# Performance work log

Hardware: AMD Instinct MI355X
Metric: run time of the kernel (lower is better)

## Reference

```python
import jax, jax.numpy as jnp
import numpy as np

N = 100000      # nodes
E = 400000      # edges per relation
R = 4           # relations
D_IN, D_HID, D_OUT = 256, 256, 128


def setup_inputs() -> dict:
    key = jax.random.key(0)
    ks = jax.random.split(key, 6)
    x = jax.random.normal(ks[0], (N, D_IN), jnp.float32)
    src = jax.random.randint(ks[1], (R, E), 0, N)
    dst = jax.random.randint(ks[2], (R, E), 0, N)
    # glorot-ish init for per-relation GraphConv weights
    W1 = jax.random.normal(ks[3], (R, D_IN, D_HID), jnp.float32) * (1.0 / np.sqrt(D_IN))
    b1 = jnp.zeros((R, D_HID), jnp.float32)
    W2 = jax.random.normal(ks[4], (R, D_HID, D_OUT), jnp.float32) * (1.0 / np.sqrt(D_HID))
    b2 = jnp.zeros((R, D_OUT), jnp.float32)
    return {"x": x, "src": src, "dst": dst, "W1": W1, "b1": b1, "W2": W2, "b2": b2}


def _rel_graphconv(x, src, dst, W, b):
    """DGL GraphConv with norm='both': D_dst^{-1/2} A D_src^{-1/2} X W + b.
    x: [N, din]; src/dst: [E]; W: [din, dout]; b: [dout]."""
    n = x.shape[0]
    xw = x @ W                                                   # [N, dout]
    ones = jnp.ones(src.shape, jnp.float32)
    out_deg = jnp.maximum(jax.ops.segment_sum(ones, src, num_segments=n), 1.0)
    in_deg = jnp.maximum(jax.ops.segment_sum(ones, dst, num_segments=n), 1.0)
    msg = xw[src] * (out_deg[src] ** -0.5)[:, None]              # [E, dout] gather + src-norm
    agg = jax.ops.segment_sum(msg, dst, num_segments=n)          # [N, dout] scatter-add
    return agg * (in_deg ** -0.5)[:, None] + b


def _hetero_layer(x, src, dst, W, b):
    # HeteroGraphConv(aggregate='sum'): run GraphConv per relation, sum results.
    conv = jax.vmap(_rel_graphconv, in_axes=(None, 0, 0, 0, 0))
    return jnp.sum(conv(x, src, dst, W, b), axis=0)              # [N, dout]


def reference(x, src, dst, W1, b1, W2, b2):
    h = jax.nn.relu(_hetero_layer(x, src, dst, W1, b1))
    return _hetero_layer(h, src, dst, W2, b2)
```

## Files before the change

### kernel.cpp

```cpp
#include <hip/hip_runtime.h>


#define RELS 4
#define DIN 256
#define DHID 256
#define DOUT 128

typedef short short8 __attribute__((ext_vector_type(8)));
typedef unsigned short ushort8 __attribute__((ext_vector_type(8)));
typedef float f32x4 __attribute__((ext_vector_type(4)));
typedef unsigned int uint4v __attribute__((ext_vector_type(4)));


__device__ __forceinline__ unsigned short f2bf(float f) {
    unsigned int u = __float_as_uint(f);
    u += 0x7FFFu + ((u >> 16) & 1u);
    return (unsigned short)(u >> 16);
}
__device__ __forceinline__ unsigned int cvt_pk_bf16(float lo, float hi) {
    unsigned int r;
    asm("v_cvt_pk_bf16_f32 %0, %1, %2" : "=v"(r) : "v"(lo), "v"(hi));
    return r;
}


__global__ void hist_kernel(const int* __restrict__ src, const int* __restrict__ dst,
                            int* __restrict__ cnt_src, int* __restrict__ cnt_dst,
                            int* __restrict__ rank, int E, int N) {
    int i = blockIdx.x * blockDim.x + threadIdx.x;
    int j = i * 4;
    if (j >= RELS * E) return;
    int4 sv = *(const int4*)(src + j);
    int4 dv = *(const int4*)(dst + j);
    int r0 = j / E, r1 = (j + 1) / E, r2 = (j + 2) / E, r3 = (j + 3) / E;
    atomicAdd(cnt_src + (size_t)r0 * N + sv.x, 1);
    atomicAdd(cnt_src + (size_t)r1 * N + sv.y, 1);
    atomicAdd(cnt_src + (size_t)r2 * N + sv.z, 1);
    atomicAdd(cnt_src + (size_t)r3 * N + sv.w, 1);
    int rk0 = atomicAdd(cnt_dst + (size_t)r0 * N + dv.x, 1);
    int rk1 = atomicAdd(cnt_dst + (size_t)r1 * N + dv.y, 1);
    int rk2 = atomicAdd(cnt_dst + (size_t)r2 * N + dv.z, 1);
    int rk3 = atomicAdd(cnt_dst + (size_t)r3 * N + dv.w, 1);
    *(int4*)(rank + j) = make_int4(rk0, rk1, rk2, rk3);
}

__global__ void scan_norm(const int* __restrict__ counts, int* __restrict__ out,
                          int* __restrict__ blk_sums, int n, int SB,
                          const int* __restrict__ cnt, float* __restrict__ nrm, long nnorm) {
    if ((int)blockIdx.x < SB) {
        __shared__ int sh[256];
        int i = blockIdx.x * 256 + threadIdx.x;
        int v = (i < n) ? counts[i] : 0;
        sh[threadIdx.x] = v;
        __syncthreads();
#pragma unroll
        for (int off = 1; off < 256; off <<= 1) {
            int t = (threadIdx.x >= off) ? sh[threadIdx.x - off] : 0;
            __syncthreads();
            sh[threadIdx.x] += t;
            __syncthreads();
        }
        if (i < n) out[i] = sh[threadIdx.x] - v;
        if (threadIdx.x == 255) blk_sums[blockIdx.x] = sh[255];
    } else {
        long i = (long)(blockIdx.x - SB) * 256 + threadIdx.x;
        if (i < nnorm) nrm[i] = rsqrtf(fmaxf((float)cnt[i], 1.0f));
    }
}

__global__ void scan_sums(int* __restrict__ bs, int nb) {
    __shared__ int sh[256];
    __shared__ int carry;
    if (threadIdx.x == 0) carry = 0;
    __syncthreads();
    for (int base = 0; base < nb; base += 256) {
        int i = base + threadIdx.x;
        int v = (i < nb) ? bs[i] : 0;
        sh[threadIdx.x] = v;
        __syncthreads();
#pragma unroll
        for (int off = 1; off < 256; off <<= 1) {
            int t = (threadIdx.x >= off) ? sh[threadIdx.x - off] : 0;
            __syncthreads();
            sh[threadIdx.x] += t;
            __syncthreads();
        }
        if (i < nb) bs[i] = sh[threadIdx.x] - v + carry;
        int tot = sh[255];
        __syncthreads();
        if (threadIdx.x == 255) carry += tot;
        __syncthreads();
    }
}

__global__ void scan_add(int* __restrict__ out, const int* __restrict__ blk_sums,
                         int n, int total) {
    int i = blockIdx.x * 256 + threadIdx.x;
    if (i < n) out[i] += blk_sums[blockIdx.x];
    if (i == n - 1) out[n] = total;
}

__global__ void fill_kernel(const int* __restrict__ src, const int* __restrict__ dst,
                            const float* __restrict__ nsrc, const int* __restrict__ row_ptr,
                            const int* __restrict__ rank, int2* __restrict__ e_pack,
                            int E, int N) {
    int i = blockIdx.x * blockDim.x + threadIdx.x;
    int j = i * 4;
    if (j >= RELS * E) return;
    int4 sv = *(const int4*)(src + j);
    int4 dv = *(const int4*)(dst + j);
    int4 rk = *(const int4*)(rank + j);
    int r0 = j / E, r1 = (j + 1) / E, r2 = (j + 2) / E, r3 = (j + 3) / E;
    int pos0 = row_ptr[(size_t)r0 * N + dv.x] + rk.x;
    int pos1 = row_ptr[(size_t)r1 * N + dv.y] + rk.y;
    int pos2 = row_ptr[(size_t)r2 * N + dv.z] + rk.z;
    int pos3 = row_ptr[(size_t)r3 * N + dv.w] + rk.w;
    e_pack[pos0] = make_int2(sv.x, __float_as_int(nsrc[(size_t)r0 * N + sv.x]));
    e_pack[pos1] = make_int2(sv.y, __float_as_int(nsrc[(size_t)r1 * N + sv.y]));
    e_pack[pos2] = make_int2(sv.z, __float_as_int(nsrc[(size_t)r2 * N + sv.z]));
    e_pack[pos3] = make_int2(sv.w, __float_as_int(nsrc[(size_t)r3 * N + sv.w]));
}


__global__ void prep_fused(const float* __restrict__ x, const float* __restrict__ W1,
                           const float* __restrict__ W2, const float* __restrict__ b1,
                           const float* __restrict__ b2,
                           unsigned short* __restrict__ x_bf, unsigned short* __restrict__ w1t,
                           unsigned short* __restrict__ w2t,
                           float* __restrict__ b1s, float* __restrict__ b2s,
                           int4* __restrict__ cnt_zero, long nz, long n8x) {
    const int T1 = RELS * DIN * DHID;
    const int T2 = RELS * DHID * DOUT;
    long i = blockIdx.x * (long)blockDim.x + threadIdx.x;
    if (i < nz) {
        cnt_zero[i] = make_int4(0, 0, 0, 0);
        return;
    }
    i -= nz;
    if (i < n8x) {
        const float4* ip = (const float4*)(x + i * 8);
        float4 v0 = ip[0], v1 = ip[1];
        ushort4 o0 = make_ushort4(f2bf(v0.x), f2bf(v0.y), f2bf(v0.z), f2bf(v0.w));
        ushort4 o1 = make_ushort4(f2bf(v1.x), f2bf(v1.y), f2bf(v1.z), f2bf(v1.w));
        ushort4* op = (ushort4*)(x_bf + i * 8);
        op[0] = o0; op[1] = o1;
    } else if (i < n8x + T1) {
        int j = (int)(i - n8x);
        int r = j / (DIN * DHID);
        int rem = j - r * (DIN * DHID);
        int k = rem / DHID, n = rem - k * DHID;
        w1t[(size_t)n * (RELS * DIN) + r * DIN + k] = f2bf(W1[j]);
    } else if (i < n8x + T1 + T2) {
        int j = (int)(i - n8x - T1);
        int r = j / (DHID * DOUT);
        int rem = j - r * (DHID * DOUT);
        int k = rem / DOUT, n = rem - k * DOUT;
        w2t[((size_t)r * DOUT + n) * DHID + k] = f2bf(W2[j]);
    } else if (i < n8x + T1 + T2 + DHID + DOUT) {
        int c = (int)(i - n8x - T1 - T2);
        if (c < DHID) {
            b1s[c] = b1[c] + b1[DHID + c] + b1[2 * DHID + c] + b1[3 * DHID + c];
        } else {
            int cc = c - DHID;
            b2s[cc] = b2[cc] + b2[DOUT + cc] + b2[2 * DOUT + cc] + b2[3 * DOUT + cc];
        }
    }
}


__device__ __forceinline__ void gload_lds16(const void* g, void* l) {
    __builtin_amdgcn_global_load_lds(
        (const __attribute__((address_space(1))) void*)g,
        (__attribute__((address_space(3))) void*)l, 16, 0, 0);
}


__global__ __launch_bounds__(512) void gemm1_k1024(
    const unsigned short* __restrict__ A, const unsigned short* __restrict__ Bt,
    unsigned short* __restrict__ C, int M, const float* __restrict__ b1s) {
    __shared__ unsigned short smA[128 * 32];
    __shared__ unsigned short smB[256 * 32];
    const int tid = threadIdx.x;
    const int lane = tid & 63;
    const int wid = tid >> 6;
    const int wr = wid >> 2, wc = wid & 3;
    const int brow = blockIdx.x * 128;
    const int K = RELS * DIN;

    f32x4 acc[4][4] = {};
    const int s = lane >> 4;
    const int rl = lane & 15;

    for (int k0 = 0; k0 < K; k0 += 32) {
        {
            int c = tid;
            int cl = c ^ ((c >> 3) & 3);
            int row = cl >> 2, slot = cl & 3;
            int ga = brow + row; ga = ga < M ? ga : M - 1;
            size_t ldsoff = (size_t)(tid & ~63) * 16;
            gload_lds16(A + (size_t)ga * K + k0 + slot * 8, (char*)smA + ldsoff);
        }
#pragma unroll
        for (int q = 0; q < 2; ++q) {
            int c = q * 512 + tid;
            int cl = c ^ ((c >> 3) & 3);
            int row = cl >> 2, slot = cl & 3;
            size_t ldsoff = (size_t)(q * 512 + (tid & ~63)) * 16;
            gload_lds16(Bt + (size_t)row * K + k0 + slot * 8, (char*)smB + ldsoff);
        }
        asm volatile("s_waitcnt vmcnt(0)" ::: "memory");
        __syncthreads();

        short8 a[4], b[4];
#pragma unroll
        for (int i = 0; i < 4; ++i) {
            int r = wr * 64 + i * 16 + rl;
            int ch = r * 4 + (s ^ ((r >> 1) & 3));
            a[i] = *(const short8*)((const char*)smA + ch * 16);
        }
#pragma unroll
        for (int j = 0; j < 4; ++j) {
            int r = wc * 64 + j * 16 + rl;
            int ch = r * 4 + (s ^ ((r >> 1) & 3));
            b[j] = *(const short8*)((const char*)smB + ch * 16);
        }
#pragma unroll
        for (int i = 0; i < 4; ++i)
#pragma unroll
            for (int j = 0; j < 4; ++j)
                acc[i][j] = __builtin_amdgcn_mfma_f32_16x16x32_bf16(a[i], b[j], acc[i][j], 0, 0, 0);
        __syncthreads();
    }

    const int rq = lane >> 4;
#pragma unroll
    for (int i = 0; i < 4; ++i) {
        int rbase = brow + wr * 64 + i * 16 + rq * 4;
#pragma unroll
        for (int j = 0; j < 4; ++j) {
            int col = wc * 64 + j * 16 + rl;
            float bb = b1s[col];
#pragma unroll
            for (int t = 0; t < 4; ++t) {
                int row = rbase + t;
                if (row < M) C[(size_t)row * DHID + col] = f2bf(fmaxf(acc[i][j][t] + bb, 0.f));
            }
        }
    }
}


__global__ __launch_bounds__(512) void gemm2_k256(
    const unsigned short* __restrict__ A, const unsigned short* __restrict__ Bt,
    unsigned short* __restrict__ C, int M,
    const float* __restrict__ nsrc_all, int Nnodes) {
    __shared__ unsigned short smA[128 * 32];
    __shared__ unsigned short smB[256 * 32];
    const int tid = threadIdx.x;
    const int lane = tid & 63;
    const int wid = tid >> 6;
    const int wr = wid >> 2, wc = wid & 3;
    const int brow = blockIdx.x * 128;
    const int bcol = blockIdx.y * 256;
    const int K = DHID;

    f32x4 acc[4][4] = {};
    const int s = lane >> 4;
    const int rl = lane & 15;

    for (int k0 = 0; k0 < K; k0 += 32) {
        {
            int c = tid;
            int cl = c ^ ((c >> 3) & 3);
            int row = cl >> 2, slot = cl & 3;
            int ga = brow + row; ga = ga < M ? ga : M - 1;
            size_t ldsoff = (size_t)(tid & ~63) * 16;
            gload_lds16(A + (size_t)ga * K + k0 + slot * 8, (char*)smA + ldsoff);
        }
#pragma unroll
        for (int q = 0; q < 2; ++q) {
            int c = q * 512 + tid;
            int cl = c ^ ((c >> 3) & 3);
            int row = cl >> 2, slot = cl & 3;
            size_t ldsoff = (size_t)(q * 512 + (tid & ~63)) * 16;
            gload_lds16(Bt + (size_t)(bcol + row) * K + k0 + slot * 8, (char*)smB + ldsoff);
        }
        asm volatile("s_waitcnt vmcnt(0)" ::: "memory");
        __syncthreads();

        short8 a[4], b[4];
#pragma unroll
        for (int i = 0; i < 4; ++i) {
            int r = wr * 64 + i * 16 + rl;
            int ch = r * 4 + (s ^ ((r >> 1) & 3));
            a[i] = *(const short8*)((const char*)smA + ch * 16);
        }
#pragma unroll
        for (int j = 0; j < 4; ++j) {
            int r = wc * 64 + j * 16 + rl;
            int ch = r * 4 + (s ^ ((r >> 1) & 3));
            b[j] = *(const short8*)((const char*)smB + ch * 16);
        }
#pragma unroll
        for (int i = 0; i < 4; ++i)
#pragma unroll
            for (int j = 0; j < 4; ++j)
                acc[i][j] = __builtin_amdgcn_mfma_f32_16x16x32_bf16(a[i], b[j], acc[i][j], 0, 0, 0);
        __syncthreads();
    }

    const int rq = lane >> 4;
#pragma unroll
    for (int i = 0; i < 4; ++i) {
        int rbase = brow + wr * 64 + i * 16 + rq * 4;
#pragma unroll
        for (int j = 0; j < 4; ++j) {
            int colg = bcol + wc * 64 + j * 16 + rl;
            const float* nsr = nsrc_all + (size_t)(colg >> 7) * Nnodes;
#pragma unroll
            for (int t = 0; t < 4; ++t) {
                int row = rbase + t;
                if (row < M)
                    C[(size_t)row * (RELS * DOUT) + colg] = f2bf(acc[i][j][t] * nsr[row]);
            }
        }
    }
}


__global__ void gather1_agg(const unsigned short* __restrict__ x_bf,
                            const int* __restrict__ rp, const int2* __restrict__ e_pack,
                            const float* __restrict__ ndst,
                            unsigned short* __restrict__ agg4, int N) {
    long w = (blockIdx.x * (long)blockDim.x + threadIdx.x) >> 6;
    int d = (int)(w >> 2);
    if (d >= N) return;
    int r = (int)(w & 3);
    int lane = threadIdx.x & 63;
    int h = lane >> 5, l = lane & 31;
    int beg = rp[(size_t)r * N + d], end = rp[(size_t)r * N + d + 1];
    float acc0[8] = {}, acc1[8] = {};
    int e = beg + h;
    for (; e + 2 < end; e += 4) {
        int2 p0 = e_pack[e];
        int2 p1 = e_pack[e + 2];
        uint4v u0 = *(const uint4v*)(x_bf + (size_t)p0.x * DIN + l * 8);
        uint4v u1 = *(const uint4v*)(x_bf + (size_t)p1.x * DIN + l * 8);
        float ns0 = __int_as_float(p0.y);
        float ns1 = __int_as_float(p1.y);
#pragma unroll
        for (int q = 0; q < 4; ++q) {
            acc0[2 * q]     += ns0 * __uint_as_float(u0[q] << 16);
            acc0[2 * q + 1] += ns0 * __uint_as_float(u0[q] & 0xffff0000u);
            acc1[2 * q]     += ns1 * __uint_as_float(u1[q] << 16);
            acc1[2 * q + 1] += ns1 * __uint_as_float(u1[q] & 0xffff0000u);
        }
    }
    if (e < end) {
        int2 p0 = e_pack[e];
        uint4v u0 = *(const uint4v*)(x_bf + (size_t)p0.x * DIN + l * 8);
        float ns0 = __int_as_float(p0.y);
#pragma unroll
        for (int q = 0; q < 4; ++q) {
            acc0[2 * q]     += ns0 * __uint_as_float(u0[q] << 16);
            acc0[2 * q + 1] += ns0 * __uint_as_float(u0[q] & 0xffff0000u);
        }
    }
    float nd = ndst[(size_t)r * N + d];
    uint4v o;
#pragma unroll
    for (int q = 0; q < 4; ++q) {
        float a = acc0[2 * q] + acc1[2 * q];
        float b = acc0[2 * q + 1] + acc1[2 * q + 1];
        a += __shfl_xor(a, 32);
        b += __shfl_xor(b, 32);
        o[q] = cvt_pk_bf16(nd * a, nd * b);
    }
    if (h == 0)
        __builtin_nontemporal_store(o, (uint4v*)(agg4 + (size_t)d * (RELS * DIN) + r * DIN + l * 8));
}

__global__ void gather2_fused(const unsigned short* __restrict__ hw4,
                              const int* __restrict__ rp, const int2* __restrict__ e_pack,
                              const float* __restrict__ ndst, const float* __restrict__ b2s,
                              float* __restrict__ out, int N) {
    int wid = (int)((blockIdx.x * (long)blockDim.x + threadIdx.x) >> 6);
    if (wid >= N) return;
    int lane = threadIdx.x & 63;
    int q = lane >> 4, l4 = lane & 15;
    float oacc[8] = {};
#pragma unroll
    for (int r = 0; r < RELS; ++r) {
        int beg = rp[(size_t)r * N + wid], end = rp[(size_t)r * N + wid + 1];
        float acc[8] = {};
        for (int e = beg + q; e < end; e += 4) {
            int s = e_pack[e].x;
            uint4v u = *(const uint4v*)(hw4 + (size_t)s * (RELS * DOUT) + r * DOUT + l4 * 8);
#pragma unroll
            for (int k = 0; k < 4; ++k) {
                acc[2 * k]     += __uint_as_float(u[k] << 16);
                acc[2 * k + 1] += __uint_as_float(u[k] & 0xffff0000u);
            }
        }
        float nd = ndst[(size_t)r * N + wid];
#pragma unroll
        for (int j = 0; j < 8; ++j) oacc[j] += nd * acc[j];
    }
#pragma unroll
    for (int j = 0; j < 8; ++j) {
        oacc[j] += __shfl_xor(oacc[j], 16);
        oacc[j] += __shfl_xor(oacc[j], 32);
    }
    if (q == 0) {
        f32x4 o0, o1;
#pragma unroll
        for (int k = 0; k < 4; ++k) o0[k] = oacc[k] + b2s[l4 * 8 + k];
#pragma unroll
        for (int k = 0; k < 4; ++k) o1[k] = oacc[4 + k] + b2s[l4 * 8 + 4 + k];
        __builtin_nontemporal_store(o0, (f32x4*)(out + (size_t)wid * DOUT + l4 * 8));
        __builtin_nontemporal_store(o1, (f32x4*)(out + (size_t)wid * DOUT + l4 * 8 + 4));
    }
}


extern "C" void kernel_launch(void* const* d_in, const int* in_sizes, int n_in,
                              void* d_out, int out_size, void* d_ws, size_t ws_size,
                              hipStream_t stream) {
    const float* x   = (const float*)d_in[0];
    const int*   src = (const int*)d_in[1];
    const int*   dst = (const int*)d_in[2];
    const float* W1  = (const float*)d_in[3];
    const float* b1  = (const float*)d_in[4];
    const float* W2  = (const float*)d_in[5];
    const float* b2  = (const float*)d_in[6];
    float* out = (float*)d_out;

    const int N = in_sizes[0] / DIN;
    const int E = in_sizes[1] / RELS;
    const int RN = RELS * N;

    char* p = (char*)d_ws;
    int*   cnt_src = (int*)p;    p += (size_t)RN * sizeof(int);
    int*   cnt_dst = (int*)p;    p += (size_t)RN * sizeof(int);
    float* nsrc    = (float*)p;  p += (size_t)RN * sizeof(float);
    float* ndst    = (float*)p;  p += (size_t)RN * sizeof(float);
    int*   row_ptr = (int*)p;    p += ((size_t)RN + 16) * sizeof(int);
    int*   rank    = (int*)p;    p += (size_t)RELS * E * sizeof(int);
    int2*  e_pack  = (int2*)p;   p += (size_t)RELS * E * sizeof(int2);
    int*   blk_sums= (int*)p;    p += 2048 * sizeof(int);
    float* b1s     = (float*)p;  p += DHID * sizeof(float);
    float* b2s     = (float*)p;  p += DOUT * sizeof(float);
    unsigned short* x_bf = (unsigned short*)p; p += (size_t)N * DIN * sizeof(short);
    unsigned short* w1t  = (unsigned short*)p; p += (size_t)RELS * DIN * DHID * sizeof(short);
    unsigned short* w2t  = (unsigned short*)p; p += (size_t)RELS * DHID * DOUT * sizeof(short);
    unsigned short* h_bf = (unsigned short*)p; p += (size_t)N * DHID * sizeof(short);
    unsigned short* agg4 = (unsigned short*)p; p += (size_t)N * RELS * DIN * sizeof(short);
    unsigned short* hw4  = agg4;

    const long n8x = (long)N * DIN / 8;
    const long nz = ((long)2 * RN + 3) / 4;
    {
        long tot = nz + n8x + RELS * DIN * DHID + RELS * DHID * DOUT + DHID + DOUT;
        prep_fused<<<(int)((tot + 255) / 256), 256, 0, stream>>>(
            x, W1, W2, b1, b2, x_bf, w1t, w2t, b1s, b2s, (int4*)cnt_src, nz, n8x);
    }

    {
        int quads = (RELS * E + 3) / 4;
        hist_kernel<<<(quads + 255) / 256, 256, 0, stream>>>(
            src, dst, cnt_src, cnt_dst, rank, E, N);
    }

    const int nscan = (RN + 255) / 256;
    {
        long nnorm = (long)2 * RN;
        int NB = (int)((nnorm + 255) / 256);
        scan_norm<<<nscan + NB, 256, 0, stream>>>(
            cnt_dst, row_ptr, blk_sums, RN, nscan, cnt_src, nsrc, nnorm);
    }
    scan_sums<<<1, 256, 0, stream>>>(blk_sums, nscan);
    scan_add<<<nscan, 256, 0, stream>>>(row_ptr, blk_sums, RN, RELS * E);

    {
        int quads = (RELS * E + 3) / 4;
        fill_kernel<<<(quads + 255) / 256, 256, 0, stream>>>(
            src, dst, nsrc, row_ptr, rank, e_pack, E, N);
    }

    const int gx = (N + 127) / 128;

    {
        long waves = (long)RELS * N;
        int blocks = (int)((waves + 3) / 4);
        gather1_agg<<<blocks, 256, 0, stream>>>(x_bf, row_ptr, e_pack, ndst, agg4, N);
        gemm1_k1024<<<gx, 512, 0, stream>>>(agg4, w1t, h_bf, N, b1s);
    }

    {
        dim3 grid(gx, 2);
        gemm2_k256<<<grid, 512, 0, stream>>>(h_bf, w2t, hw4, N, nsrc, N);
        int gblocks = (N + 3) / 4;
        gather2_fused<<<gblocks, 256, 0, stream>>>(hw4, row_ptr, e_pack, ndst, b2s, out, N);
    }
}
```

Baseline: 673.5 us.

## Fuse layer-1 gather aggregation with GEMM via shared-memory tile

Replaces the separate gather1_agg kernel and the K=1024 GEMM with one kernel. Each 64-row block aggregates neighbor features per relation into an LDS tile and immediately multiplies it with that relation's weight slice, accumulating across relations. This removes the round trip of the N x 1024 bf16 intermediate through global memory. In exchange, B operands are read directly from global memory without LDS staging, and gather and MFMA phases are serialized within each block with barriers, which may lower occupancy and overlap.

```diff
diff --git a/kernel.cpp b/kernel.cpp
--- a/kernel.cpp
+++ b/kernel.cpp
@@ -5,6 +5,7 @@
 #define DIN 256
 #define DHID 256
 #define DOUT 128
+#define LDP 264
 
 typedef short short8 __attribute__((ext_vector_type(8)));
 typedef unsigned short ushort8 __attribute__((ext_vector_type(8)));
@@ -175,67 +176,101 @@
 }
 
 
-__global__ __launch_bounds__(512) void gemm1_k1024(
-    const unsigned short* __restrict__ A, const unsigned short* __restrict__ Bt,
-    unsigned short* __restrict__ C, int M, const float* __restrict__ b1s) {
-    __shared__ unsigned short smA[128 * 32];
-    __shared__ unsigned short smB[256 * 32];
+__global__ __launch_bounds__(512, 8) void fused1(
+    const unsigned short* __restrict__ x_bf, const int* __restrict__ rp,
+    const int2* __restrict__ e_pack, const float* __restrict__ ndst,
+    const unsigned short* __restrict__ w1t, const float* __restrict__ b1s,
+    unsigned short* __restrict__ h_bf, int N) {
+    __shared__ __align__(16) unsigned short smA[64 * LDP];
     const int tid = threadIdx.x;
     const int lane = tid & 63;
     const int wid = tid >> 6;
     const int wr = wid >> 2, wc = wid & 3;
-    const int brow = blockIdx.x * 128;
-    const int K = RELS * DIN;
-
-    f32x4 acc[4][4] = {};
-    const int s = lane >> 4;
-    const int rl = lane & 15;
-
-    for (int k0 = 0; k0 < K; k0 += 32) {
-        {
-            int c = tid;
-            int cl = c ^ ((c >> 3) & 3);
-            int row = cl >> 2, slot = cl & 3;
-            int ga = brow + row; ga = ga < M ? ga : M - 1;
-            size_t ldsoff = (size_t)(tid & ~63) * 16;
-            gload_lds16(A + (size_t)ga * K + k0 + slot * 8, (char*)smA + ldsoff);
-        }
-#pragma unroll
-        for (int q = 0; q < 2; ++q) {
-            int c = q * 512 + tid;
-            int cl = c ^ ((c >> 3) & 3);
-            int row = cl >> 2, slot = cl & 3;
-            size_t ldsoff = (size_t)(q * 512 + (tid & ~63)) * 16;
-            gload_lds16(Bt + (size_t)row * K + k0 + slot * 8, (char*)smB + ldsoff);
-        }
-        asm volatile("s_waitcnt vmcnt(0)" ::: "memory");
-        __syncthreads();
-
-        short8 a[4], b[4];
-#pragma unroll
-        for (int i = 0; i < 4; ++i) {
-            int r = wr * 64 + i * 16 + rl;
-            int ch = r * 4 + (s ^ ((r >> 1) & 3));
-            a[i] = *(const short8*)((const char*)smA + ch * 16);
-        }
-#pragma unroll
-        for (int j = 0; j < 4; ++j) {
-            int r = wc * 64 + j * 16 + rl;
-            int ch = r * 4 + (s ^ ((r >> 1) & 3));
-            b[j] = *(const short8*)((const char*)smB + ch * 16);
-        }
-#pragma unroll
-        for (int i = 0; i < 4; ++i)
-#pragma unroll
-            for (int j = 0; j < 4; ++j)
-                acc[i][j] = __builtin_amdgcn_mfma_f32_16x16x32_bf16(a[i], b[j], acc[i][j], 0, 0, 0);
+    const int brow = blockIdx.x * 64;
+    const int s = lane >> 4, rl = lane & 15;
+    const int h = lane >> 5, l = lane & 31;
+
+    f32x4 acc[2][4] = {};
+
+    for (int r = 0; r < RELS; ++r) {
+        for (int t = 0; t < 8; ++t) {
+            int row = wid * 8 + t;
+            int node = brow + row;
+            int beg = 0, end = 0;
+            float nd = 0.f;
+            if (node < N) {
+                size_t base = (size_t)r * N + node;
+                beg = rp[base]; end = rp[base + 1];
+                nd = ndst[base];
+            }
+            float acc0[8] = {}, acc1[8] = {};
+            int e = beg + h;
+            for (; e + 2 < end; e += 4) {
+                int2 p0 = e_pack[e];
+                int2 p1 = e_pack[e + 2];
+                uint4v u0 = *(const uint4v*)(x_bf + (size_t)p0.x * DIN + l * 8);
+                uint4v u1 = *(const uint4v*)(x_bf + (size_t)p1.x * DIN + l * 8);
+                float ns0 = __int_as_float(p0.y);
+                float ns1 = __int_as_float(p1.y);
+#pragma unroll
+                for (int q = 0; q < 4; ++q) {
+                    acc0[2 * q]     += ns0 * __uint_as_float(u0[q] << 16);
+                    acc0[2 * q + 1] += ns0 * __uint_as_float(u0[q] & 0xffff0000u);
+                    acc1[2 * q]     += ns1 * __uint_as_float(u1[q] << 16);
+                    acc1[2 * q + 1] += ns1 * __uint_as_float(u1[q] & 0xffff0000u);
+                }
+            }
+            if (e < end) {
+                int2 p0 = e_pack[e];
+                uint4v u0 = *(const uint4v*)(x_bf + (size_t)p0.x * DIN + l * 8);
+                float ns0 = __int_as_float(p0.y);
+#pragma unroll
+                for (int q = 0; q < 4; ++q) {
+                    acc0[2 * q]     += ns0 * __uint_as_float(u0[q] << 16);
+                    acc0[2 * q + 1] += ns0 * __uint_as_float(u0[q] & 0xffff0000u);
+                }
+            }
+            uint4v o;
+#pragma unroll
+            for (int q = 0; q < 4; ++q) {
+                float a = acc0[2 * q] + acc1[2 * q];
+                float b = acc0[2 * q + 1] + acc1[2 * q + 1];
+                a += __shfl_xor(a, 32);
+                b += __shfl_xor(b, 32);
+                o[q] = cvt_pk_bf16(nd * a, nd * b);
+            }
+            if (h == 0)
+                *(uint4v*)(smA + (size_t)row * LDP + l * 8) = o;
+        }
+        __syncthreads();
+
+        const unsigned short* wb = w1t + (size_t)r * DIN;
+#pragma unroll 2
+        for (int k0 = 0; k0 < 256; k0 += 32) {
+            short8 a[2], b[4];
+#pragma unroll
+            for (int i = 0; i < 2; ++i) {
+                int arow = wr * 32 + i * 16 + rl;
+                a[i] = *(const short8*)(smA + (size_t)arow * LDP + k0 + s * 8);
+            }
+#pragma unroll
+            for (int j = 0; j < 4; ++j) {
+                int col = wc * 64 + j * 16 + rl;
+                b[j] = *(const short8*)(wb + (size_t)col * (RELS * DIN) + k0 + s * 8);
+            }
+#pragma unroll
+            for (int i = 0; i < 2; ++i)
+#pragma unroll
+                for (int j = 0; j < 4; ++j)
+                    acc[i][j] = __builtin_amdgcn_mfma_f32_16x16x32_bf16(a[i], b[j], acc[i][j], 0, 0, 0);
+        }
         __syncthreads();
     }
 
     const int rq = lane >> 4;
 #pragma unroll
-    for (int i = 0; i < 4; ++i) {
-        int rbase = brow + wr * 64 + i * 16 + rq * 4;
+    for (int i = 0; i < 2; ++i) {
+        int rbase = brow + wr * 32 + i * 16 + rq * 4;
 #pragma unroll
         for (int j = 0; j < 4; ++j) {
             int col = wc * 64 + j * 16 + rl;
@@ -243,7 +278,7 @@
 #pragma unroll
             for (int t = 0; t < 4; ++t) {
                 int row = rbase + t;
-                if (row < M) C[(size_t)row * DHID + col] = f2bf(fmaxf(acc[i][j][t] + bb, 0.f));
+                if (row < N) h_bf[(size_t)row * DHID + col] = f2bf(fmaxf(acc[i][j][t] + bb, 0.f));
             }
         }
     }
@@ -327,58 +362,6 @@
     }
 }
 
-
-__global__ void gather1_agg(const unsigned short* __restrict__ x_bf,
-                            const int* __restrict__ rp, const int2* __restrict__ e_pack,
-                            const float* __restrict__ ndst,
-                            unsigned short* __restrict__ agg4, int N) {
-    long w = (blockIdx.x * (long)blockDim.x + threadIdx.x) >> 6;
-    int d = (int)(w >> 2);
-    if (d >= N) return;
-    int r = (int)(w & 3);
-    int lane = threadIdx.x & 63;
-    int h = lane >> 5, l = lane & 31;
-    int beg = rp[(size_t)r * N + d], end = rp[(size_t)r * N + d + 1];
-    float acc0[8] = {}, acc1[8] = {};
-    int e = beg + h;
-    for (; e + 2 < end; e += 4) {
-        int2 p0 = e_pack[e];
-        int2 p1 = e_pack[e + 2];
-        uint4v u0 = *(const uint4v*)(x_bf + (size_t)p0.x * DIN + l * 8);
-        uint4v u1 = *(const uint4v*)(x_bf + (size_t)p1.x * DIN + l * 8);
-        float ns0 = __int_as_float(p0.y);
-        float ns1 = __int_as_float(p1.y);
-#pragma unroll
-        for (int q = 0; q < 4; ++q) {
-            acc0[2 * q]     += ns0 * __uint_as_float(u0[q] << 16);
-            acc0[2 * q + 1] += ns0 * __uint_as_float(u0[q] & 0xffff0000u);
-            acc1[2 * q]     += ns1 * __uint_as_float(u1[q] << 16);
-            acc1[2 * q + 1] += ns1 * __uint_as_float(u1[q] & 0xffff0000u);
-        }
-    }
-    if (e < end) {
-        int2 p0 = e_pack[e];
-        uint4v u0 = *(const uint4v*)(x_bf + (size_t)p0.x * DIN + l * 8);
-        float ns0 = __int_as_float(p0.y);
-#pragma unroll
-        for (int q = 0; q < 4; ++q) {
-            acc0[2 * q]     += ns0 * __uint_as_float(u0[q] << 16);
-            acc0[2 * q + 1] += ns0 * __uint_as_float(u0[q] & 0xffff0000u);
-        }
-    }
-    float nd = ndst[(size_t)r * N + d];
-    uint4v o;
-#pragma unroll
-    for (int q = 0; q < 4; ++q) {
-        float a = acc0[2 * q] + acc1[2 * q];
-        float b = acc0[2 * q + 1] + acc1[2 * q + 1];
-        a += __shfl_xor(a, 32);
-        b += __shfl_xor(b, 32);
-        o[q] = cvt_pk_bf16(nd * a, nd * b);
-    }
-    if (h == 0)
-        __builtin_nontemporal_store(o, (uint4v*)(agg4 + (size_t)d * (RELS * DIN) + r * DIN + l * 8));
-}
 
 __global__ void gather2_fused(const unsigned short* __restrict__ hw4,
                               const int* __restrict__ rp, const int2* __restrict__ e_pack,
@@ -454,8 +437,7 @@
     unsigned short* w1t  = (unsigned short*)p; p += (size_t)RELS * DIN * DHID * sizeof(short);
     unsigned short* w2t  = (unsigned short*)p; p += (size_t)RELS * DHID * DOUT * sizeof(short);
     unsigned short* h_bf = (unsigned short*)p; p += (size_t)N * DHID * sizeof(short);
-    unsigned short* agg4 = (unsigned short*)p; p += (size_t)N * RELS * DIN * sizeof(short);
-    unsigned short* hw4  = agg4;
+    unsigned short* hw4  = (unsigned short*)p; p += (size_t)N * RELS * DOUT * sizeof(short);
 
     const long n8x = (long)N * DIN / 8;
     const long nz = ((long)2 * RN + 3) / 4;
@@ -487,16 +469,13 @@
             src, dst, nsrc, row_ptr, rank, e_pack, E, N);
     }
 
-    const int gx = (N + 127) / 128;
-
-    {
-        long waves = (long)RELS * N;
-        int blocks = (int)((waves + 3) / 4);
-        gather1_agg<<<blocks, 256, 0, stream>>>(x_bf, row_ptr, e_pack, ndst, agg4, N);
-        gemm1_k1024<<<gx, 512, 0, stream>>>(agg4, w1t, h_bf, N, b1s);
-    }
-
-    {
+    {
+        int gx64 = (N + 63) / 64;
+        fused1<<<gx64, 512, 0, stream>>>(x_bf, row_ptr, e_pack, ndst, w1t, b1s, h_bf, N);
+    }
+
+    {
+        const int gx = (N + 127) / 128;
         dim3 grid(gx, 2);
         gemm2_k256<<<grid, 512, 0, stream>>>(h_bf, w2t, hw4, N, nsrc, N);
         int gblocks = (N + 3) / 4;
```

After: 790.5 us. 1.17x slower.
